# Performance work log

Measured on AMD Instinct MI355X. Metric: run time of the kernel, lower is better.

## Reference

```python
import jax, jax.numpy as jnp
import numpy as np

# Dimensions (source globals scaled to production: r=256 residues, s=128 sequences)
S, R, CM, CZ, C, H = 128, 256, 256, 128, 32, 8
EPS = 1e-5  # torch LayerNorm default


def setup_inputs() -> dict:
    key = jax.random.key(0)
    ks = jax.random.split(key, 14)
    msa = jax.random.normal(ks[0], (S, R, CM), dtype=jnp.float32)
    pair = jax.random.normal(ks[1], (R, R, CZ), dtype=jnp.float32)
    u = lambda k, shape, fan: jax.random.uniform(k, shape, jnp.float32, -1.0 / np.sqrt(fan), 1.0 / np.sqrt(fan))
    return {
        "msa": msa,
        "pair": pair,
        # per-head LayerNorm affine params (stacked over head axis)
        "ln_msa_g": 1.0 + 0.1 * jax.random.normal(ks[2], (H, CM), dtype=jnp.float32),
        "ln_msa_b": 0.1 * jax.random.normal(ks[3], (H, CM), dtype=jnp.float32),
        "ln_pair_g": 1.0 + 0.1 * jax.random.normal(ks[4], (H, CZ), dtype=jnp.float32),
        "ln_pair_b": 0.1 * jax.random.normal(ks[5], (H, CZ), dtype=jnp.float32),
        # per-head projections (torch Linear without bias; stored as (in, out))
        "Wq": u(ks[6], (H, CM, C), CM),
        "Wk": u(ks[7], (H, CM, C), CM),
        "Wv": u(ks[8], (H, CM, C), CM),
        "Wg": u(ks[9], (H, CM, C), CM),
        "Wb": u(ks[10], (H, CZ, S), CZ),  # linear_b: c_z -> s
        # output projection c*H -> c_m (with bias)
        "Wo": u(ks[11], (H * C, CM), H * C),
        "bo": u(ks[12], (CM,), H * C),
    }


def _forward(msa, pair, ln_msa_g, ln_msa_b, ln_pair_g, ln_pair_b, Wq, Wk, Wv, Wg, Wb, Wo, bo):
    # LayerNorm normalization is head-independent; only affine differs per head.
    mu = msa.mean(-1, keepdims=True)
    var = msa.var(-1, keepdims=True)
    nm = (msa - mu) * jax.lax.rsqrt(var + EPS)              # (S, R, CM)
    p = nm[None] * ln_msa_g[:, None, None, :] + ln_msa_b[:, None, None, :]  # (H, S, R, CM)

    q = jnp.einsum("hsrc,hcd->hsrd", p, Wq)                  # (H, S, R, C)
    k = jnp.einsum("hsrc,hcd->hsrd", p, Wk)
    v = jnp.einsum("hsrc,hcd->hsrd", p, Wv)
    g = jax.nn.sigmoid(jnp.einsum("hsrc,hcd->hsrd", p, Wg))

    pmu = pair.mean(-1, keepdims=True)
    pvar = pair.var(-1, keepdims=True)
    npair = (pair - pmu) * jax.lax.rsqrt(pvar + EPS)         # (R, R, CZ)
    pp = npair[None] * ln_pair_g[:, None, None, :] + ln_pair_b[:, None, None, :]  # (H, R, R, CZ)
    bflat = jnp.einsum("hijc,hcs->hijs", pp, Wb)             # (H, R, R, S)
    # Faithful to torch: b = linear_b(flat_pair).view(s, r, r) -- a raw
    # row-major reinterpretation (NOT a transpose).
    b = bflat.reshape(H, S, R, R)

    inv_sqrt_c = np.float32(1.0 / np.sqrt(C))
    scores = (jnp.einsum("hsid,hsjd->hsij", q, k) + b) * inv_sqrt_c  # (H, S, R, R)
    # Source softmax is over dim=-2 (the query/row axis), faithful here.
    a = jax.nn.softmax(scores, axis=-2)
    o = g * jnp.einsum("hsij,hsjd->hsid", a, v)              # (H, S, R, C)

    # concat heads on last dim: (S, R, H*C)
    cat = jnp.transpose(o, (1, 2, 0, 3)).reshape(S, R, H * C)
    return cat @ Wo + bo                                      # (S, R, CM)


def reference(msa, pair, ln_msa_g, ln_msa_b, ln_pair_g, ln_pair_b, Wq, Wk, Wv, Wg, Wb, Wo, bo):
    return _forward(msa, pair, ln_msa_g, ln_msa_b, ln_pair_g, ln_pair_b, Wq, Wk, Wv, Wg, Wb, Wo, bo)
```

## Files before the change

kernel.cpp:

```cpp
#include <hip/hip_runtime.h>
#include <hip/hip_bf16.h>


namespace {
constexpr int S_ = 128, R_ = 256, CM_ = 256, CZ_ = 128, C_ = 32, H_ = 8;
constexpr int SR_ = S_ * R_;
constexpr int RR_ = R_ * R_;
constexpr float EPS_ = 1e-5f;
constexpr float ISC_ = 0.17677669529663687f;

constexpr size_t OFF_WC  = 0;
constexpr size_t OFF_BC  = 131072;
constexpr size_t OFF_BBP = 132096;
constexpr size_t F32_END = 133120;
constexpr size_t BF_BASE = F32_END * 4;
constexpr size_t QKVG_ELEMS  = (size_t)H_ * SR_ * C_;
constexpr size_t CAT_ELEMS   = (size_t)SR_ * CM_;
constexpr size_t WBT_ELEMS   = (size_t)H_ * 128 * 128;
constexpr size_t WOT_ELEMS   = (size_t)256 * 256;
constexpr size_t PAIRN_ELEMS = (size_t)RR_ * 128;
constexpr size_t MSAN_ELEMS  = (size_t)SR_ * 256;
constexpr size_t NEED_BYTES =
    BF_BASE +
    (4 * QKVG_ELEMS + CAT_ELEMS + WBT_ELEMS + WOT_ELEMS + PAIRN_ELEMS + MSAN_ELEMS) * 2;
}

typedef unsigned short bf_t;
typedef short s8v __attribute__((ext_vector_type(8)));
typedef float f4v __attribute__((ext_vector_type(4)));

__device__ __forceinline__ unsigned pk2(float lo, float hi) {
  __hip_bfloat162 t = __float22bfloat162_rn(float2{lo, hi});
  return *reinterpret_cast<unsigned*>(&t);
}
__device__ __forceinline__ bf_t pk1(float v) {
  __hip_bfloat16 t = __float2bfloat16(v);
  return *reinterpret_cast<bf_t*>(&t);
}
__device__ __forceinline__ float uplo(unsigned u) { return __uint_as_float(u << 16); }
__device__ __forceinline__ f4v mfma16(s8v a, s8v b, f4v c) {
  return __builtin_amdgcn_mfma_f32_16x16x32_bf16(a, b, c, 0, 0, 0);
}
__device__ __forceinline__ s8v ld8(const bf_t* p) { return *reinterpret_cast<const s8v*>(p); }

__global__ __launch_bounds__(512) void prep_all_k(
    const float* __restrict__ pair, const float* __restrict__ msa,
    const float* __restrict__ lng_m, const float* __restrict__ lnb_m,
    const float* __restrict__ lng_p, const float* __restrict__ lnb_p,
    const float* __restrict__ Wq, const float* __restrict__ Wk, const float* __restrict__ Wv,
    const float* __restrict__ Wg, const float* __restrict__ Wb, const float* __restrict__ Wo,
    bf_t* __restrict__ pairN, bf_t* __restrict__ msaN, bf_t* __restrict__ wct,
    bf_t* __restrict__ wbt, bf_t* __restrict__ wot, float* __restrict__ bc,
    float* __restrict__ bbp) {
  int b = blockIdx.x;
  int tid = threadIdx.x;
  int lane = tid & 63;
  if (b < 4) {
    int ob = b * 4 + (tid >> 7);
    int t = tid & 127;
    if (ob < H_) {
      int h = ob;
      int m = t >> 5, d = t & 31;
      const float* Wsrc = (m == 0) ? Wq : (m == 1) ? Wk : (m == 2) ? Wv : Wg;
      float scale = (m == 0) ? ISC_ : 1.0f;
      float bias = 0.f;
      for (int c = 0; c < CM_; c++)
        bias += lnb_m[h * CM_ + c] * Wsrc[((size_t)h * CM_ + c) * C_ + d];
      bc[h * 128 + t] = bias * scale;
    } else {
      int h = ob - H_;
      float bias = 0.f;
      for (int c = 0; c < CZ_; c++)
        bias += lnb_p[h * CZ_ + c] * Wb[((size_t)h * CZ_ + c) * S_ + t];
      bbp[h * 128 + t] = bias * ISC_;
    }
  } else if (b < 8196) {
    int row = (b - 4) * 8 + (tid >> 6);
    float2 v = reinterpret_cast<const float2*>(pair + (size_t)row * CZ_)[lane];
    float s = v.x + v.y;
    float s2 = v.x * v.x + v.y * v.y;
    for (int off = 32; off; off >>= 1) {
      s += __shfl_xor(s, off);
      s2 += __shfl_xor(s2, off);
    }
    float m = s / CZ_;
    float rs = rsqrtf(s2 / CZ_ - m * m + EPS_);
    reinterpret_cast<unsigned*>(pairN)[(size_t)row * 64 + lane] =
        pk2((v.x - m) * rs, (v.y - m) * rs);
  } else if (b < 12292) {
    int row = (b - 8196) * 8 + (tid >> 6);
    float4 v = reinterpret_cast<const float4*>(msa + (size_t)row * CM_)[lane];
    float s = v.x + v.y + v.z + v.w;
    float s2 = v.x * v.x + v.y * v.y + v.z * v.z + v.w * v.w;
    for (int off = 32; off; off >>= 1) {
      s += __shfl_xor(s, off);
      s2 += __shfl_xor(s2, off);
    }
    float m = s / CM_;
    float rs = rsqrtf(s2 / CM_ - m * m + EPS_);
    uint2 wv;
    wv.x = pk2((v.x - m) * rs, (v.y - m) * rs);
    wv.y = pk2((v.z - m) * rs, (v.w - m) * rs);
    reinterpret_cast<uint2*>(msaN)[(size_t)row * 64 + lane] = wv;
  } else {
    int idx = (b - 12292) * 512 + tid;
    if (idx < 262144) {
      int h = idx >> 15, rem = idx & 32767;
      int j = rem >> 8, c = rem & 255;
      int m = j >> 5, d = j & 31;
      const float* Wsrc = (m == 0) ? Wq : (m == 1) ? Wk : (m == 2) ? Wv : Wg;
      float scale = (m == 0) ? ISC_ : 1.0f;
      wct[idx] = pk1(lng_m[h * CM_ + c] * Wsrc[((size_t)h * CM_ + c) * C_ + d] * scale);
    } else if (idx < 262144 + 131072) {
      int i2 = idx - 262144;
      int h = i2 >> 14, rem = i2 & 16383;
      int t = rem >> 7, c = rem & 127;
      wbt[i2] = pk1(lng_p[h * CZ_ + c] * Wb[((size_t)h * CZ_ + c) * S_ + t] * ISC_);
    } else {
      int i3 = idx - 262144 - 131072;
      int n = i3 >> 8, k = i3 & 255;
      wot[i3] = pk1(Wo[(size_t)k * 256 + n]);
    }
  }
}

__global__ __launch_bounds__(512, 1) void qkvg_mfma_k(
    const bf_t* __restrict__ msaN, const bf_t* __restrict__ wct, const float* __restrict__ bc,
    bf_t* __restrict__ q, bf_t* __restrict__ k, bf_t* __restrict__ v, bf_t* __restrict__ g) {
  __shared__ bf_t sm_a[128 * 256];
  __shared__ bf_t sm_w[128 * 256];
  int ib = blockIdx.x;
  int tid = threadIdx.x;
  int w = tid >> 6, l = tid & 63;
  int l15 = l & 15, l4 = l >> 4;
  int iw = w >> 2, jw = w & 3;
  int sr0 = ib * 128;
  int sx7 = l15 & 7;
#pragma unroll
  for (int rep = 0; rep < 8; rep++) {
    int flat = rep * 512 + tid;
    int row = flat >> 5, c = flat & 31;
    *reinterpret_cast<uint4*>(&sm_a[row * 256 + ((c ^ (row & 7)) << 3)]) =
        *reinterpret_cast<const uint4*>(msaN + (size_t)(sr0 + row) * 256 + c * 8);
  }
  for (int h = 0; h < H_; h++) {
    __syncthreads();
#pragma unroll
    for (int rep = 0; rep < 8; rep++) {
      int flat = rep * 512 + tid;
      int row = flat >> 5, c = flat & 31;
      *reinterpret_cast<uint4*>(&sm_w[row * 256 + ((c ^ (row & 7)) << 3)]) =
          *reinterpret_cast<const uint4*>(wct + ((size_t)h * 128 + row) * 256 + c * 8);
    }
    f4v acc[4][2];
#pragma unroll
    for (int jt = 0; jt < 2; jt++) {
      float bb = bc[h * 128 + jw * 32 + jt * 16 + l15];
#pragma unroll
      for (int it = 0; it < 4; it++) acc[it][jt] = f4v{bb, bb, bb, bb};
    }
    __syncthreads();
#pragma unroll
    for (int ks = 0; ks < 8; ks++) {
      int ch = ks * 4 + l4;
      s8v a[4], b[2];
#pragma unroll
      for (int it = 0; it < 4; it++)
        a[it] = ld8(&sm_a[(iw * 64 + it * 16 + l15) * 256 + ((ch ^ sx7) << 3)]);
#pragma unroll
      for (int jt = 0; jt < 2; jt++)
        b[jt] = ld8(&sm_w[(jw * 32 + jt * 16 + l15) * 256 + ((ch ^ sx7) << 3)]);
#pragma unroll
      for (int it = 0; it < 4; it++)
#pragma unroll
        for (int jt = 0; jt < 2; jt++) acc[it][jt] = mfma16(a[it], b[jt], acc[it][jt]);
    }
#pragma unroll
    for (int it = 0; it < 4; it++) {
#pragma unroll
      for (int jt = 0; jt < 2; jt++) {
        int j = jw * 32 + jt * 16 + l15;
        int m_ = j >> 5, d = j & 31;
        bf_t* dst = (m_ == 0) ? q : (m_ == 1) ? k : (m_ == 2) ? v : g;
#pragma unroll
        for (int r = 0; r < 4; r++) {
          int i = iw * 64 + it * 16 + l4 * 4 + r;
          float val = acc[it][jt][r];
          if (m_ == 3) val = 1.f / (1.f + __expf(-val));
          dst[((size_t)h * SR_ + sr0 + i) * C_ + d] = pk1(val);
        }
      }
    }
  }
}

__global__ __launch_bounds__(512, 2) void attn_mfma_k(
    const bf_t* __restrict__ pairN, const bf_t* __restrict__ wbt,
    const float* __restrict__ bbp, const bf_t* __restrict__ qg, const bf_t* __restrict__ kg,
    const bf_t* __restrict__ vg, const bf_t* __restrict__ gg, bf_t* __restrict__ cat) {
  __shared__ bf_t sm_pn[256 * 64];
  __shared__ bf_t sm_wt[64 * 64];
  __shared__ bf_t sm_p[256 * 64];
  __shared__ bf_t sm_vt[32 * 64];
  __shared__ float sm_redm[4 * 64];
  __shared__ float sm_reds[4 * 64];

  int b = blockIdx.x;
  int x = b & 7, tq = b >> 3;
  int round = tq >> 5, inner = tq & 31;
  int sl = inner >> 3, h = inner & 7;
  int s = (round * 8 + x) * 4 + sl;

  int tid = threadIdx.x;
  int w = tid >> 6, l = tid & 63;
  int l15 = l & 15, l4 = l >> 4, sx7 = l15 & 7;
  int iw = w >> 1, jw = w & 1, dw = w & 1;
  size_t base = ((size_t)h * SR_ + (size_t)s * R_) * C_;
  const bf_t* wbh = wbt + (size_t)h * 128 * 128;

  s8v qa[4];
#pragma unroll
  for (int it = 0; it < 4; it++)
    qa[it] = ld8(&qg[base + (size_t)(iw * 64 + it * 16 + l15) * C_ + l4 * 8]);

  f4v accO[4];
#pragma unroll
  for (int it = 0; it < 4; it++) accO[it] = f4v{0.f, 0.f, 0.f, 0.f};

  for (int pass = 0; pass < 4; pass++) {
    int p = pass >> 1, jh = pass & 1;
    int j0 = p * 128 + jh * 64;
    s8v kb0 = ld8(&kg[base + (size_t)(j0 + jw * 32 + l15) * C_ + l4 * 8]);
    s8v kb1 = ld8(&kg[base + (size_t)(j0 + jw * 32 + 16 + l15) * C_ + l4 * 8]);
    __syncthreads();
    if (tid >= 256) {
      int t2 = tid - 256;
      int j = t2 >> 2, dc = t2 & 3;
      uint4 u = *reinterpret_cast<const uint4*>(vg + base + (size_t)(j0 + j) * C_ + dc * 8);
      unsigned uu[4] = {u.x, u.y, u.z, u.w};
#pragma unroll
      for (int e = 0; e < 8; e++) {
        int d = dc * 8 + e;
        bf_t val = (bf_t)((uu[e >> 1] >> ((e & 1) * 16)) & 0xffff);
        sm_vt[d * 64 + ((((j >> 3) ^ (d & 7)) << 3) + (j & 7))] = val;
      }
    }
    f4v acc[4][2];
    {
      float bb0 = bbp[h * 128 + jh * 64 + jw * 32 + l15];
      float bb1 = bbp[h * 128 + jh * 64 + jw * 32 + 16 + l15];
#pragma unroll
      for (int it = 0; it < 4; it++) {
        acc[it][0] = f4v{bb0, bb0, bb0, bb0};
        acc[it][1] = f4v{bb1, bb1, bb1, bb1};
      }
    }
#pragma unroll
    for (int kc = 0; kc < 2; kc++) {
#pragma unroll
      for (int rep = 0; rep < 4; rep++) {
        int idx = rep * 512 + tid;
        int row = idx >> 3, c8 = idx & 7;
        int gr = (2 * s + (row >> 7)) * 256 + 2 * (row & 127) + p;
        *reinterpret_cast<uint4*>(&sm_pn[row * 64 + ((c8 ^ (row & 7)) << 3)]) =
            *reinterpret_cast<const uint4*>(pairN + (size_t)gr * 128 + kc * 64 + c8 * 8);
      }
      {
        int row = tid >> 3, c8 = tid & 7;
        *reinterpret_cast<uint4*>(&sm_wt[row * 64 + ((c8 ^ (row & 7)) << 3)]) =
            *reinterpret_cast<const uint4*>(wbh + (size_t)(jh * 64 + row) * 128 + kc * 64 +
                                            c8 * 8);
      }
      __syncthreads();
#pragma unroll
      for (int ks = 0; ks < 2; ks++) {
        int ch = ks * 4 + l4;
        s8v a[4], b2[2];
#pragma unroll
        for (int it = 0; it < 4; it++)
          a[it] = ld8(&sm_pn[(iw * 64 + it * 16 + l15) * 64 + ((ch ^ sx7) << 3)]);
#pragma unroll
        for (int u = 0; u < 2; u++)
          b2[u] = ld8(&sm_wt[(jw * 32 + u * 16 + l15) * 64 + ((ch ^ sx7) << 3)]);
#pragma unroll
        for (int it = 0; it < 4; it++) {
          acc[it][0] = mfma16(a[it], b2[0], acc[it][0]);
          acc[it][1] = mfma16(a[it], b2[1], acc[it][1]);
        }
      }
      if (kc == 0) __syncthreads();
    }
#pragma unroll
    for (int it = 0; it < 4; it++) {
      acc[it][0] = mfma16(qa[it], kb0, acc[it][0]);
      acc[it][1] = mfma16(qa[it], kb1, acc[it][1]);
    }
    float fac[2], mloc[2];
#pragma unroll
    for (int u = 0; u < 2; u++) {
      float m0 = -1e30f;
#pragma unroll
      for (int it = 0; it < 4; it++)
#pragma unroll
        for (int r = 0; r < 4; r++) m0 = fmaxf(m0, acc[it][u][r]);
      m0 = fmaxf(m0, __shfl_xor(m0, 16));
      m0 = fmaxf(m0, __shfl_xor(m0, 32));
      float s0 = 0.f;
#pragma unroll
      for (int it = 0; it < 4; it++)
#pragma unroll
        for (int r = 0; r < 4; r++) {
          float e = __expf(acc[it][u][r] - m0);
          acc[it][u][r] = e;
          s0 += e;
        }
      s0 += __shfl_xor(s0, 16);
      s0 += __shfl_xor(s0, 32);
      mloc[u] = m0;
      if (l < 16) {
        sm_redm[iw * 64 + jw * 32 + u * 16 + l] = m0;
        sm_reds[iw * 64 + jw * 32 + u * 16 + l] = s0;
      }
    }
    __syncthreads();
#pragma unroll
    for (int u = 0; u < 2; u++) {
      int jc = jw * 32 + u * 16 + l15;
      float M = fmaxf(fmaxf(sm_redm[jc], sm_redm[64 + jc]),
                      fmaxf(sm_redm[128 + jc], sm_redm[192 + jc]));
      float tot = 0.f;
#pragma unroll
      for (int gx = 0; gx < 4; gx++)
        tot += sm_reds[gx * 64 + jc] * __expf(sm_redm[gx * 64 + jc] - M);
      fac[u] = __expf(mloc[u] - M) / tot;
#pragma unroll
      for (int it = 0; it < 4; it++)
#pragma unroll
        for (int r = 0; r < 4; r++) {
          int i = iw * 64 + it * 16 + l4 * 4 + r;
          sm_p[i * 64 + ((((jc >> 3) ^ (i & 7)) << 3) + (jc & 7))] =
              pk1(acc[it][u][r] * fac[u]);
        }
    }
    __syncthreads();
#pragma unroll
    for (int ks = 0; ks < 2; ks++) {
      int ch = ks * 4 + l4;
      s8v vb = ld8(&sm_vt[(dw * 16 + l15) * 64 + ((ch ^ sx7) << 3)]);
#pragma unroll
      for (int it = 0; it < 4; it++) {
        s8v pa = ld8(&sm_p[(iw * 64 + it * 16 + l15) * 64 + ((ch ^ sx7) << 3)]);
        accO[it] = mfma16(pa, vb, accO[it]);
      }
    }
  }
#pragma unroll
  for (int it = 0; it < 4; it++) {
#pragma unroll
    for (int r = 0; r < 4; r++) {
      int i = iw * 64 + it * 16 + l4 * 4 + r;
      int d = dw * 16 + l15;
      float gf = uplo((unsigned)gg[base + (size_t)i * C_ + d]);
      cat[((size_t)s * R_ + i) * 256 + h * 32 + d] = pk1(accO[it][r] * gf);
    }
  }
}

__global__ __launch_bounds__(512, 1) void out_mfma_k(const bf_t* __restrict__ cat,
                                                     const bf_t* __restrict__ wot,
                                                     const float* __restrict__ bo,
                                                     float* __restrict__ out) {
  __shared__ bf_t sm_a[128 * 256];
  __shared__ bf_t sm_b[128 * 256];
  int ib = blockIdx.x;
  int tid = threadIdx.x;
  int w = tid >> 6, l = tid & 63;
  int l15 = l & 15, l4 = l >> 4, sx7 = l15 & 7;
  int iw = w >> 2, jw = w & 3;
  int sr0 = ib * 128;
#pragma unroll
  for (int rep = 0; rep < 8; rep++) {
    int flat = rep * 512 + tid;
    int row = flat >> 5, c = flat & 31;
    *reinterpret_cast<uint4*>(&sm_a[row * 256 + ((c ^ (row & 7)) << 3)]) =
        *reinterpret_cast<const uint4*>(cat + (size_t)(sr0 + row) * 256 + c * 8);
  }
  for (int nb = 0; nb < 2; nb++) {
    __syncthreads();
#pragma unroll
    for (int rep = 0; rep < 8; rep++) {
      int flat = rep * 512 + tid;
      int row = flat >> 5, c = flat & 31;
      *reinterpret_cast<uint4*>(&sm_b[row * 256 + ((c ^ (row & 7)) << 3)]) =
          *reinterpret_cast<const uint4*>(wot + (size_t)(nb * 128 + row) * 256 + c * 8);
    }
    f4v acc[4][2];
#pragma unroll
    for (int jt = 0; jt < 2; jt++) {
      float bb = bo[nb * 128 + jw * 32 + jt * 16 + l15];
#pragma unroll
      for (int it = 0; it < 4; it++) acc[it][jt] = f4v{bb, bb, bb, bb};
    }
    __syncthreads();
#pragma unroll
    for (int ks = 0; ks < 8; ks++) {
      int ch = ks * 4 + l4;
      s8v a[4], b[2];
#pragma unroll
      for (int it = 0; it < 4; it++)
        a[it] = ld8(&sm_a[(iw * 64 + it * 16 + l15) * 256 + ((ch ^ sx7) << 3)]);
#pragma unroll
      for (int jt = 0; jt < 2; jt++)
        b[jt] = ld8(&sm_b[(jw * 32 + jt * 16 + l15) * 256 + ((ch ^ sx7) << 3)]);
#pragma unroll
      for (int it = 0; it < 4; it++)
#pragma unroll
        for (int jt = 0; jt < 2; jt++) acc[it][jt] = mfma16(a[it], b[jt], acc[it][jt]);
    }
#pragma unroll
    for (int it = 0; it < 4; it++)
#pragma unroll
      for (int jt = 0; jt < 2; jt++) {
        int n = nb * 128 + jw * 32 + jt * 16 + l15;
#pragma unroll
        for (int r = 0; r < 4; r++) {
          int i = iw * 64 + it * 16 + l4 * 4 + r;
          out[(size_t)(sr0 + i) * 256 + n] = acc[it][jt][r];
        }
      }
  }
}

extern "C" void kernel_launch(void* const* d_in, const int* in_sizes, int n_in, void* d_out,
                              int out_size, void* d_ws, size_t ws_size, hipStream_t stream) {
  if (ws_size < NEED_BYTES) return;

  const float* msa = (const float*)d_in[0];
  const float* pair = (const float*)d_in[1];
  const float* lng_m = (const float*)d_in[2];
  const float* lnb_m = (const float*)d_in[3];
  const float* lng_p = (const float*)d_in[4];
  const float* lnb_p = (const float*)d_in[5];
  const float* Wq = (const float*)d_in[6];
  const float* Wk = (const float*)d_in[7];
  const float* Wv = (const float*)d_in[8];
  const float* Wg = (const float*)d_in[9];
  const float* Wb = (const float*)d_in[10];
  const float* Wo = (const float*)d_in[11];
  const float* bo = (const float*)d_in[12];
  float* out = (float*)d_out;
  float* ws = (float*)d_ws;

  bf_t* wct = (bf_t*)(ws + OFF_WC);
  float* bc = ws + OFF_BC;
  float* bbp = ws + OFF_BBP;
  bf_t* qb = (bf_t*)((char*)d_ws + BF_BASE);
  bf_t* kb = qb + QKVG_ELEMS;
  bf_t* vb = kb + QKVG_ELEMS;
  bf_t* gb = vb + QKVG_ELEMS;
  bf_t* cat = gb + QKVG_ELEMS;
  bf_t* wbt = cat + CAT_ELEMS;
  bf_t* wot = wbt + WBT_ELEMS;
  bf_t* pairN = wot + WOT_ELEMS;
  bf_t* msaN = pairN + PAIRN_ELEMS;

  prep_all_k<<<13188, 512, 0, stream>>>(pair, msa, lng_m, lnb_m, lng_p, lnb_p, Wq, Wk, Wv, Wg,
                                        Wb, Wo, pairN, msaN, wct, wbt, wot, bc, bbp);
  qkvg_mfma_k<<<SR_ / 128, 512, 0, stream>>>(msaN, wct, bc, qb, kb, vb, gb);
  attn_mfma_k<<<S_ * H_, 512, 0, stream>>>(pairN, wbt, bbp, qb, kb, vb, gb, cat);
  out_mfma_k<<<SR_ / 128, 512, 0, stream>>>(cat, wot, bo, out);
}
```

Before: 157.5 us.

## Widen attention column tile to 128 so each pair tile is loaded once

The attention kernel now handles 128 key columns per pass instead of 64, cutting the pass count from four to two. Each normalized pair tile is staged into shared memory once rather than twice, and the K, V and bias work is done in larger chunks. In exchange, shared memory per block roughly doubles and accumulator registers grow. Launch bounds drop to one block per CU, which lowers occupancy and reduces latency hiding.

```diff
diff --git a/kernel.cpp b/kernel.cpp
--- a/kernel.cpp
+++ b/kernel.cpp
@@ -194,16 +194,16 @@
   }
 }
 
-__global__ __launch_bounds__(512, 2) void attn_mfma_k(
+__global__ __launch_bounds__(512, 1) void attn_mfma_k(
     const bf_t* __restrict__ pairN, const bf_t* __restrict__ wbt,
     const float* __restrict__ bbp, const bf_t* __restrict__ qg, const bf_t* __restrict__ kg,
     const bf_t* __restrict__ vg, const bf_t* __restrict__ gg, bf_t* __restrict__ cat) {
   __shared__ bf_t sm_pn[256 * 64];
-  __shared__ bf_t sm_wt[64 * 64];
-  __shared__ bf_t sm_p[256 * 64];
-  __shared__ bf_t sm_vt[32 * 64];
-  __shared__ float sm_redm[4 * 64];
-  __shared__ float sm_reds[4 * 64];
+  __shared__ bf_t sm_wt[128 * 64];
+  __shared__ bf_t sm_p[256 * 128];
+  __shared__ bf_t sm_vt[32 * 128];
+  __shared__ float sm_redm[4 * 128];
+  __shared__ float sm_reds[4 * 128];
 
   int b = blockIdx.x;
   int x = b & 7, tq = b >> 3;
@@ -227,33 +227,30 @@
 #pragma unroll
   for (int it = 0; it < 4; it++) accO[it] = f4v{0.f, 0.f, 0.f, 0.f};
 
-  for (int pass = 0; pass < 4; pass++) {
-    int p = pass >> 1, jh = pass & 1;
-    int j0 = p * 128 + jh * 64;
-    s8v kb0 = ld8(&kg[base + (size_t)(j0 + jw * 32 + l15) * C_ + l4 * 8]);
-    s8v kb1 = ld8(&kg[base + (size_t)(j0 + jw * 32 + 16 + l15) * C_ + l4 * 8]);
-    __syncthreads();
-    if (tid >= 256) {
-      int t2 = tid - 256;
-      int j = t2 >> 2, dc = t2 & 3;
+  for (int p = 0; p < 2; p++) {
+    int j0 = p * 128;
+    s8v kb[4];
+#pragma unroll
+    for (int jt = 0; jt < 4; jt++)
+      kb[jt] = ld8(&kg[base + (size_t)(j0 + jw * 64 + jt * 16 + l15) * C_ + l4 * 8]);
+    __syncthreads();
+    {
+      int j = tid >> 2, dc = tid & 3;
       uint4 u = *reinterpret_cast<const uint4*>(vg + base + (size_t)(j0 + j) * C_ + dc * 8);
       unsigned uu[4] = {u.x, u.y, u.z, u.w};
 #pragma unroll
       for (int e = 0; e < 8; e++) {
         int d = dc * 8 + e;
-        bf_t val = (bf_t)((uu[e >> 1] >> ((e & 1) * 16)) & 0xffff);
-        sm_vt[d * 64 + ((((j >> 3) ^ (d & 7)) << 3) + (j & 7))] = val;
-      }
-    }
-    f4v acc[4][2];
-    {
-      float bb0 = bbp[h * 128 + jh * 64 + jw * 32 + l15];
-      float bb1 = bbp[h * 128 + jh * 64 + jw * 32 + 16 + l15];
-#pragma unroll
-      for (int it = 0; it < 4; it++) {
-        acc[it][0] = f4v{bb0, bb0, bb0, bb0};
-        acc[it][1] = f4v{bb1, bb1, bb1, bb1};
-      }
+        sm_vt[d * 128 + ((((j >> 3) ^ (d & 7)) << 3) + (j & 7))] =
+            (bf_t)((uu[e >> 1] >> ((e & 1) * 16)) & 0xffff);
+      }
+    }
+    f4v acc[4][4];
+#pragma unroll
+    for (int jt = 0; jt < 4; jt++) {
+      float bb = bbp[h * 128 + jw * 64 + jt * 16 + l15];
+#pragma unroll
+      for (int it = 0; it < 4; it++) acc[it][jt] = f4v{bb, bb, bb, bb};
     }
 #pragma unroll
     for (int kc = 0; kc < 2; kc++) {
@@ -265,39 +262,38 @@
         *reinterpret_cast<uint4*>(&sm_pn[row * 64 + ((c8 ^ (row & 7)) << 3)]) =
             *reinterpret_cast<const uint4*>(pairN + (size_t)gr * 128 + kc * 64 + c8 * 8);
       }
-      {
-        int row = tid >> 3, c8 = tid & 7;
+#pragma unroll
+      for (int rep = 0; rep < 2; rep++) {
+        int idx = rep * 512 + tid;
+        int row = idx >> 3, c8 = idx & 7;
         *reinterpret_cast<uint4*>(&sm_wt[row * 64 + ((c8 ^ (row & 7)) << 3)]) =
-            *reinterpret_cast<const uint4*>(wbh + (size_t)(jh * 64 + row) * 128 + kc * 64 +
-                                            c8 * 8);
+            *reinterpret_cast<const uint4*>(wbh + (size_t)row * 128 + kc * 64 + c8 * 8);
       }
       __syncthreads();
 #pragma unroll
       for (int ks = 0; ks < 2; ks++) {
         int ch = ks * 4 + l4;
-        s8v a[4], b2[2];
+        s8v a[4], b2[4];
 #pragma unroll
         for (int it = 0; it < 4; it++)
           a[it] = ld8(&sm_pn[(iw * 64 + it * 16 + l15) * 64 + ((ch ^ sx7) << 3)]);
 #pragma unroll
-        for (int u = 0; u < 2; u++)
-          b2[u] = ld8(&sm_wt[(jw * 32 + u * 16 + l15) * 64 + ((ch ^ sx7) << 3)]);
-#pragma unroll
-        for (int it = 0; it < 4; it++) {
-          acc[it][0] = mfma16(a[it], b2[0], acc[it][0]);
-          acc[it][1] = mfma16(a[it], b2[1], acc[it][1]);
-        }
+        for (int jt = 0; jt < 4; jt++)
+          b2[jt] = ld8(&sm_wt[(jw * 64 + jt * 16 + l15) * 64 + ((ch ^ sx7) << 3)]);
+#pragma unroll
+        for (int it = 0; it < 4; it++)
+#pragma unroll
+          for (int jt = 0; jt < 4; jt++) acc[it][jt] = mfma16(a[it], b2[jt], acc[it][jt]);
       }
       if (kc == 0) __syncthreads();
     }
 #pragma unroll
-    for (int it = 0; it < 4; it++) {
-      acc[it][0] = mfma16(qa[it], kb0, acc[it][0]);
-      acc[it][1] = mfma16(qa[it], kb1, acc[it][1]);
-    }
-    float fac[2], mloc[2];
-#pragma unroll
-    for (int u = 0; u < 2; u++) {
+    for (int it = 0; it < 4; it++)
+#pragma unroll
+      for (int jt = 0; jt < 4; jt++) acc[it][jt] = mfma16(qa[it], kb[jt], acc[it][jt]);
+    float fac[4], mloc[4];
+#pragma unroll
+    for (int u = 0; u < 4; u++) {
       float m0 = -1e30f;
 #pragma unroll
       for (int it = 0; it < 4; it++)
@@ -318,38 +314,38 @@
       s0 += __shfl_xor(s0, 32);
       mloc[u] = m0;
       if (l < 16) {
-        sm_redm[iw * 64 + jw * 32 + u * 16 + l] = m0;
-        sm_reds[iw * 64 + jw * 32 + u * 16 + l] = s0;
-      }
-    }
-    __syncthreads();
-#pragma unroll
-    for (int u = 0; u < 2; u++) {
-      int jc = jw * 32 + u * 16 + l15;
-      float M = fmaxf(fmaxf(sm_redm[jc], sm_redm[64 + jc]),
-                      fmaxf(sm_redm[128 + jc], sm_redm[192 + jc]));
+        sm_redm[iw * 128 + jw * 64 + u * 16 + l] = m0;
+        sm_reds[iw * 128 + jw * 64 + u * 16 + l] = s0;
+      }
+    }
+    __syncthreads();
+#pragma unroll
+    for (int u = 0; u < 4; u++) {
+      int jc = jw * 64 + u * 16 + l15;
+      float M = fmaxf(fmaxf(sm_redm[jc], sm_redm[128 + jc]),
+                      fmaxf(sm_redm[256 + jc], sm_redm[384 + jc]));
       float tot = 0.f;
 #pragma unroll
       for (int gx = 0; gx < 4; gx++)
-        tot += sm_reds[gx * 64 + jc] * __expf(sm_redm[gx * 64 + jc] - M);
+        tot += sm_reds[gx * 128 + jc] * __expf(sm_redm[gx * 128 + jc] - M);
       fac[u] = __expf(mloc[u] - M) / tot;
 #pragma unroll
       for (int it = 0; it < 4; it++)
 #pragma unroll
         for (int r = 0; r < 4; r++) {
           int i = iw * 64 + it * 16 + l4 * 4 + r;
-          sm_p[i * 64 + ((((jc >> 3) ^ (i & 7)) << 3) + (jc & 7))] =
+          sm_p[i * 128 + ((((jc >> 3) ^ (i & 7)) << 3) + (jc & 7))] =
               pk1(acc[it][u][r] * fac[u]);
         }
     }
     __syncthreads();
 #pragma unroll
-    for (int ks = 0; ks < 2; ks++) {
+    for (int ks = 0; ks < 4; ks++) {
       int ch = ks * 4 + l4;
-      s8v vb = ld8(&sm_vt[(dw * 16 + l15) * 64 + ((ch ^ sx7) << 3)]);
+      s8v vb = ld8(&sm_vt[(dw * 16 + l15) * 128 + ((ch ^ sx7) << 3)]);
 #pragma unroll
       for (int it = 0; it < 4; it++) {
-        s8v pa = ld8(&sm_p[(iw * 64 + it * 16 + l15) * 64 + ((ch ^ sx7) << 3)]);
+        s8v pa = ld8(&sm_p[(iw * 64 + it * 16 + l15) * 128 + ((ch ^ sx7) << 3)]);
         accO[it] = mfma16(pa, vb, accO[it]);
       }
     }
```

New measurement: 221.7 us. +40.7%, slower.
